# Performance work log

Measured on AMD Instinct MI355X. Metric: run time of the kernel, lower is better.

Reference implementation:

```python
import jax, jax.numpy as jnp
import numpy as np

T, H, HS, NH = 1024, 2048, 64, 32
TM, TD = 32, 64  # time-mix / time-decay LoRA dims for hidden_size != 4096


def _layernorm(x, w, b, eps=1e-5):
    mu = jnp.mean(x, axis=-1, keepdims=True)
    var = jnp.mean(jnp.square(x - mu), axis=-1, keepdims=True)
    return (x - mu) * jax.lax.rsqrt(var + eps) * w + b


def setup_inputs() -> dict:
    key = jax.random.key(0)
    ks = jax.random.split(key, 16)
    s = 0.02
    return {
        'x': jax.random.normal(ks[0], (1, T, H), jnp.float32),
        'state1': jax.random.normal(ks[1], (1, H), jnp.float32),
        'state2': jax.random.normal(ks[2], (NH, HS, HS), jnp.float32) * s,
        'ln1_w': jnp.ones((H,), jnp.float32),
        'ln1_b': jnp.zeros((H,), jnp.float32),
        'time_maa_x': jax.random.normal(ks[3], (1, 1, H), jnp.float32) * s,
        'time_maa': jax.random.normal(ks[4], (5, 1, H), jnp.float32) * s,
        'time_maa_w1': jax.random.normal(ks[5], (H, 5 * TM), jnp.float32) * s,
        'time_maa_w2': jax.random.normal(ks[6], (5, TM, H), jnp.float32) * s,
        'time_decay_w1': jax.random.normal(ks[7], (H, TD), jnp.float32) * s,
        'time_decay_w2': jax.random.normal(ks[8], (TD, H), jnp.float32) * s,
        'time_decay_p': jax.random.normal(ks[9], (NH, 1, HS), jnp.float32),
        'time_first': jax.random.normal(ks[10], (NH, 1, HS), jnp.float32) * s,
        'W_r': jax.random.normal(ks[11], (H, H), jnp.float32) * s,
        'W_k': jax.random.normal(ks[12], (H, H), jnp.float32) * s,
        'W_v': jax.random.normal(ks[13], (H, H), jnp.float32) * s,
        'W_g': jax.random.normal(ks[14], (H, H), jnp.float32) * s,
        'W_o': jax.random.normal(ks[15], (H, H), jnp.float32) * s,
        'ln_x_w': jnp.ones((H,), jnp.float32),
        'ln_x_b': jnp.zeros((H,), jnp.float32),
    }


def _forward(x, state1, state2, ln1_w, ln1_b, time_maa_x, time_maa,
             time_maa_w1, time_maa_w2, time_decay_w1, time_decay_w2,
             time_decay_p, time_first, W_r, W_k, W_v, W_g, W_o, ln_x_w, ln_x_b):
    last_x = x
    xl = _layernorm(x, ln1_w, ln1_b)                 # (1,T,H)
    Tn = xl.shape[1]
    # token shift: sx = shift(x) - x, with state1 as the t=-1 token
    past = jnp.concatenate([state1[:, None, :], xl[:, :-1, :]], axis=1)
    sx = past - xl                                    # (1,T,H)
    state1_out = xl[:, -1, :]
    # data-dependent time-mix (LoRA through w1/w2)
    xxx = xl + sx * time_maa_x                        # (1,T,H)
    t5 = jnp.tanh(xxx[0] @ time_maa_w1)               # (T,5*TM)
    t5 = t5.reshape(Tn, 5, TM).transpose(1, 0, 2)     # (5,T,TM)
    mix = jnp.einsum('ftm,fmh->fth', t5, time_maa_w2) # (5,T,H)
    x5 = xl + sx * (mix + time_maa)                   # (5,T,H)
    mw, mk, mv, mr, mg = x5[0], x5[1], x5[2], x5[3], x5[4]
    r = (mr @ W_r).reshape(Tn, NH, HS)
    k = (mk @ W_k).reshape(Tn, NH, HS)
    v = (mv @ W_v).reshape(Tn, NH, HS)
    g = jax.nn.silu(mg @ W_g)                         # (T,H)
    # data-dependent decay
    td = (jnp.tanh(mw @ time_decay_w1) @ time_decay_w2).reshape(Tn, NH, 1, HS)
    td = td + time_decay_p                            # (T,NH,1,HS)
    td = jnp.exp(-jnp.exp(jnp.clip(td, -9.72, 2.27)))
    # WKV linear-attention recurrence
    kv = jnp.einsum('thi,thj->thij', v, k)            # (T,NH,HS,HS)

    def step(s2, inp):
        kv_t, r_t, td_t = inp
        tmp = kv_t * time_first + s2                  # (NH,HS,HS)
        wkv_t = jnp.einsum('hij,hj->hi', tmp, r_t)    # (NH,HS)
        return kv_t + s2 * td_t, wkv_t

    state2_out, wkv = jax.lax.scan(step, state2, (kv, r, td))  # wkv (T,NH,HS)
    # group-norm over head dim, then affine with ln_x params at hidden width
    y = _layernorm(wkv, 1.0, 0.0).reshape(1, Tn, H)
    y = (y * ln_x_w + ln_x_b) * g[None]
    y = y @ W_o
    return last_x + y, state1_out, state2_out


def reference(x, state1, state2, ln1_w, ln1_b, time_maa_x, time_maa,
              time_maa_w1, time_maa_w2, time_decay_w1, time_decay_w2,
              time_decay_p, time_first, W_r, W_k, W_v, W_g, W_o, ln_x_w, ln_x_b):
    return _forward(x, state1, state2, ln1_w, ln1_b, time_maa_x, time_maa,
                    time_maa_w1, time_maa_w2, time_decay_w1, time_decay_w2,
                    time_decay_p, time_first, W_r, W_k, W_v, W_g, W_o, ln_x_w, ln_x_b)
```

## Files before the change

### kernel.cpp

```cpp
#include <hip/hip_runtime.h>
#include <hip/hip_bf16.h>
#include <math.h>

#define TLEN 1024
#define HDIM 2048
#define NHEAD 32
#define HSZ 64
#define THE (TLEN * HDIM)
#define NC 32
#define CT (TLEN / NC)

typedef __attribute__((ext_vector_type(8))) short bf16x8;
typedef __attribute__((ext_vector_type(4))) float f32x4;

__device__ __forceinline__ float waveRedSum(float v) {
#pragma unroll
  for (int off = 32; off > 0; off >>= 1) v += __shfl_xor(v, off, 64);
  return v;
}

__device__ __forceinline__ void gll16(const __hip_bfloat16* g, __hip_bfloat16* l) {
  __builtin_amdgcn_global_load_lds(
      (const __attribute__((address_space(1))) void*)g,
      (__attribute__((address_space(3))) void*)l, 16, 0, 0);
}

struct TrArgs {
  const float* src[8];
  __hip_bfloat16* dst[8];
  int R[8];
  int C[8];
};

__global__ __launch_bounds__(256) void transp_kernel(TrArgs ta) {
  const int z = blockIdx.z;
  const int R = ta.R[z], C = ta.C[z];
  const int c0 = blockIdx.x * 32, r0 = blockIdx.y * 32;
  if (c0 >= C || r0 >= R) return;
  __shared__ float tile[32][33];
  const int tx = threadIdx.x & 31, ty = threadIdx.x >> 5;
  const float* src = ta.src[z];
  __hip_bfloat16* dst = ta.dst[z];
#pragma unroll
  for (int i = 0; i < 4; i++)
    tile[ty + i * 8][tx] = src[(size_t)(r0 + ty + i * 8) * C + c0 + tx];
  __syncthreads();
#pragma unroll
  for (int i = 0; i < 4; i++)
    dst[(size_t)(c0 + ty + i * 8) * R + r0 + tx] = __float2bfloat16(tile[tx][ty + i * 8]);
}

__global__ __launch_bounds__(256) void ln1_kernel(const float* __restrict__ x,
                                                  const float* __restrict__ w,
                                                  const float* __restrict__ b,
                                                  float* __restrict__ xl,
                                                  float* __restrict__ s1out) {
  const int t = blockIdx.x;
  const int tid = threadIdx.x;
  const int wid = tid >> 6, lane = tid & 63;
  const float4* xr = (const float4*)(x + (size_t)t * HDIM);
  float4 a = xr[tid];
  float4 c = xr[tid + 256];
  float va[8] = {a.x, a.y, a.z, a.w, c.x, c.y, c.z, c.w};
  float sum = 0.f;
#pragma unroll
  for (int i = 0; i < 8; i++) sum += va[i];
  sum = waveRedSum(sum);
  __shared__ float red[8];
  if (lane == 0) red[wid] = sum;
  __syncthreads();
  const float mu = (red[0] + red[1] + red[2] + red[3]) * (1.f / HDIM);
  float vs = 0.f;
#pragma unroll
  for (int i = 0; i < 8; i++) { float d = va[i] - mu; vs += d * d; }
  vs = waveRedSum(vs);
  if (lane == 0) red[4 + wid] = vs;
  __syncthreads();
  const float rstd = rsqrtf((red[4] + red[5] + red[6] + red[7]) * (1.f / HDIM) + 1e-5f);
  float* xrow = xl + (size_t)t * HDIM;
#pragma unroll
  for (int i = 0; i < 8; i++) {
    const int idx = (i < 4) ? (4 * tid + i) : (1024 + 4 * tid + (i - 4));
    const float o = (va[i] - mu) * rstd * w[idx] + b[idx];
    xrow[idx] = o;
    if (t == TLEN - 1) s1out[idx] = o;
  }
}

__global__ __launch_bounds__(256) void tokshift_kernel(const float* __restrict__ xl,
                                                       const float* __restrict__ s1,
                                                       const float* __restrict__ tmx,
                                                       __hip_bfloat16* __restrict__ xxx) {
  const int t = blockIdx.x;
  const int h = blockIdx.y * 256 + threadIdx.x;
  const float cur = xl[(size_t)t * HDIM + h];
  const float past = (t > 0) ? xl[(size_t)(t - 1) * HDIM + h] : s1[h];
  xxx[(size_t)t * HDIM + h] = __float2bfloat16(cur + (past - cur) * tmx[h]);
}

__global__ __launch_bounds__(256) void mix_kernel(const float* __restrict__ t5,
                                                  const float* __restrict__ xl,
                                                  const float* __restrict__ s1,
                                                  const float* __restrict__ w2,
                                                  const float* __restrict__ maa,
                                                  __hip_bfloat16* __restrict__ x5b) {
  const int h = blockIdx.x * 256 + threadIdx.x;
  const int t0 = blockIdx.y * 8;
  __shared__ float t5L[8 * 160];
  for (int i = threadIdx.x; i < 8 * 160; i += 256) {
    const int rr = i / 160, cc = i - rr * 160;
    t5L[i] = t5[(size_t)(t0 + rr) * 160 + cc];
  }
  __syncthreads();
  float mixv[8][5];
#pragma unroll
  for (int ts = 0; ts < 8; ts++)
#pragma unroll
    for (int f = 0; f < 5; f++) mixv[ts][f] = 0.f;
#pragma unroll
  for (int f = 0; f < 5; f++) {
#pragma unroll 4
    for (int m = 0; m < 32; m++) {
      const float w2v = w2[(size_t)(f * 32 + m) * HDIM + h];
#pragma unroll
      for (int ts = 0; ts < 8; ts++) mixv[ts][f] += t5L[ts * 160 + f * 32 + m] * w2v;
    }
  }
#pragma unroll
  for (int ts = 0; ts < 8; ts++) {
    const int t = t0 + ts;
    const float cur = xl[(size_t)t * HDIM + h];
    const float past = (t > 0) ? xl[(size_t)(t - 1) * HDIM + h] : s1[h];
    const float sx = past - cur;
#pragma unroll
    for (int f = 0; f < 5; f++) {
      const float v = cur + sx * (mixv[ts][f] + maa[(size_t)f * HDIM + h]);
      x5b[(size_t)f * THE + (size_t)t * HDIM + h] = __float2bfloat16(v);
    }
  }
}

struct GemmArgs {
  const __hip_bfloat16* A[8];
  const __hip_bfloat16* B[8];
  void* C[8];
  const float* aux[8];
  int epi[8];
  int M, N, K, Ks;
};

__global__ __launch_bounds__(256) void gemm_bt(GemmArgs ga) {
  const int z = blockIdx.z;
  const __hip_bfloat16* __restrict__ A = ga.A[z];
  const __hip_bfloat16* __restrict__ Bt = ga.B[z];
  const int N = ga.N, K = ga.K, Ks = ga.Ks;
  const int epi = ga.epi[z];
  const float* __restrict__ aux = ga.aux[z];
  void* Cz = ga.C[z];

  __shared__ __align__(16) __hip_bfloat16 As[2][128 * 64];
  __shared__ __align__(16) __hip_bfloat16 Bs[2][128 * 64];

  const int tid = threadIdx.x;
  const int wid = tid >> 6;
  const int lane = tid & 63;

  int bx = blockIdx.x, by = blockIdx.y;
  if (gridDim.x == 8 && gridDim.y == 16) {
    const int flat = bx + 8 * by;
    const int xcd = flat & 7, rem = flat >> 3;
    bx = rem & 7;
    by = xcd + 8 * (rem >> 3);
  }
  const int m0 = bx * 128;
  const int n0 = by * 128;
  const int wr = wid >> 1, wc = wid & 1;

  const int srow = lane >> 3;
  const int chunkS = (lane & 7) ^ srow;
  const __hip_bfloat16* aSrcQ[4];
  const __hip_bfloat16* bSrcQ[4];
#pragma unroll
  for (int q = 0; q < 4; q++) {
    const int arow = wid * 32 + q * 8 + srow;
    int brow = n0 + arow; if (brow > N - 1) brow = N - 1;
    aSrcQ[q] = A + (size_t)(m0 + arow) * Ks + chunkS * 8;
    bSrcQ[q] = Bt + (size_t)brow * Ks + chunkS * 8;
  }

  f32x4 acc[4][4];
#pragma unroll
  for (int m = 0; m < 4; m++)
#pragma unroll
    for (int n = 0; n < 4; n++) acc[m][n] = 0.f;

  const int lr = lane & 15;
  const int cbase = lane >> 4;
  int aoffk[2], boffk[2];
#pragma unroll
  for (int kg = 0; kg < 2; kg++) {
    const int phys = (kg * 4 + cbase) ^ (lr & 7);
    aoffk[kg] = (wr * 64 + lr) * 64 + phys * 8;
    boffk[kg] = (wc * 64 + lr) * 64 + phys * 8;
  }

#define STAGE(BUF, KT)                                              \
  do {                                                              \
    _Pragma("unroll") for (int q = 0; q < 4; q++) {                 \
      gll16(aSrcQ[q] + (KT), &As[BUF][(wid * 32 + q * 8) * 64]);    \
      gll16(bSrcQ[q] + (KT), &Bs[BUF][(wid * 32 + q * 8) * 64]);    \
    }                                                               \
  } while (0)

  STAGE(0, 0);
  int cur = 0;
  for (int kt = 0; kt < K; kt += 64) {
    const bool more = (kt + 64 < K);
    if (more) {
      STAGE(cur ^ 1, kt + 64);
      asm volatile("s_waitcnt vmcnt(8)" ::: "memory");
    } else {
      asm volatile("s_waitcnt vmcnt(0)" ::: "memory");
    }
    __builtin_amdgcn_s_barrier();
#pragma unroll
    for (int kg = 0; kg < 2; kg++) {
      bf16x8 af[4], bfv[4];
#pragma unroll
      for (int m = 0; m < 4; m++) af[m] = *(const bf16x8*)&As[cur][aoffk[kg] + m * 16 * 64];
#pragma unroll
      for (int n = 0; n < 4; n++) bfv[n] = *(const bf16x8*)&Bs[cur][boffk[kg] + n * 16 * 64];
#pragma unroll
      for (int m = 0; m < 4; m++)
#pragma unroll
        for (int n = 0; n < 4; n++)
          acc[m][n] = __builtin_amdgcn_mfma_f32_16x16x32_bf16(af[m], bfv[n], acc[m][n], 0, 0, 0);
    }
    __builtin_amdgcn_s_barrier();
    cur ^= 1;
  }
#undef STAGE

  const int r4 = (lane >> 4) * 4;
#pragma unroll
  for (int m = 0; m < 4; m++) {
#pragma unroll
    for (int n = 0; n < 4; n++) {
      const int gn = n0 + wc * 64 + n * 16 + lr;
      if (gn < N) {
#pragma unroll
        for (int r = 0; r < 4; r++) {
          const int gm = m0 + wr * 64 + m * 16 + r4 + r;
          const size_t idx = (size_t)gm * N + gn;
          const float v = acc[m][n][r];
          switch (epi) {
            case 0: ((__hip_bfloat16*)Cz)[idx] = __float2bfloat16(v); break;
            case 1: ((__hip_bfloat16*)Cz)[idx] = __float2bfloat16(v / (1.f + expf(-v))); break;
            case 2: ((float*)Cz)[idx] = tanhf(v); break;
            case 3: ((__hip_bfloat16*)Cz)[idx] = __float2bfloat16(tanhf(v)); break;
            case 4: {
              float wv = v + aux[gn];
              wv = fminf(fmaxf(wv, -9.72f), 2.27f);
              ((float*)Cz)[idx] = expf(-expf(wv));
            } break;
            case 5: ((float*)Cz)[idx] = v + aux[idx]; break;
            case 6: ((float*)Cz)[idx] = v; break;
          }
        }
      }
    }
  }
}

__global__ __launch_bounds__(256) void comb8_tanh_f32(const float* __restrict__ p,
                                                      float* __restrict__ o, int n) {
  const int i = blockIdx.x * 256 + threadIdx.x;
  float s = 0.f;
#pragma unroll
  for (int k = 0; k < 8; k++) s += p[(size_t)k * n + i];
  o[i] = tanhf(s);
}

__global__ __launch_bounds__(256) void comb8_tanh_bf16(const float* __restrict__ p,
                                                       __hip_bfloat16* __restrict__ o, int n) {
  const int i = blockIdx.x * 256 + threadIdx.x;
  float s = 0.f;
#pragma unroll
  for (int k = 0; k < 8; k++) s += p[(size_t)k * n + i];
  o[i] = __float2bfloat16(tanhf(s));
}

__global__ __launch_bounds__(256) void comb2_resid(const float* __restrict__ p,
                                                   const float* __restrict__ x,
                                                   float* __restrict__ o) {
  const int i = blockIdx.x * 256 + threadIdx.x;
  const float4 a = ((const float4*)p)[i];
  const float4 b = ((const float4*)(p + THE))[i];
  const float4 c = ((const float4*)x)[i];
  ((float4*)o)[i] = make_float4(a.x + b.x + c.x, a.y + b.y + c.y,
                                a.z + b.z + c.z, a.w + b.w + c.w);
}

__global__ __launch_bounds__(64) void decay_kernel(const __hip_bfloat16* __restrict__ rb,
                                                   const float* __restrict__ td,
                                                   __hip_bfloat16* __restrict__ rt,
                                                   float* __restrict__ Ptot) {
  const int blk = blockIdx.x;
  const int c = blk >> 5, h = blk & 31;
  const int j = threadIdx.x;
  const int hb = h * HSZ;
  const int t0 = c * CT;
  float A = 1.f;
  for (int t = 0; t < CT; t++) {
    const size_t rowb = (size_t)(t0 + t) * HDIM + hb;
    rt[(((size_t)c * NHEAD + h) * CT + t) * HSZ + j] =
        __float2bfloat16(__bfloat162float(rb[rowb + j]) * A);
    A *= td[rowb + j];
  }
  Ptot[((size_t)c * NHEAD + h) * HSZ + j] = A;
}

__global__ __launch_bounds__(256) void scan_local_kernel(const __hip_bfloat16* __restrict__ kb,
                                                         const __hip_bfloat16* __restrict__ rb,
                                                         const float* __restrict__ td,
                                                         const __hip_bfloat16* __restrict__ vb,
                                                         float* __restrict__ wkv,
                                                         float* __restrict__ qT) {
  const int blk = blockIdx.x;
  const int c = blk >> 5, h = blk & 31;
  const int w = threadIdx.x >> 6;
  const int i = threadIdx.x & 63;
  __shared__ float plds[2][4][64];

  float s[16];
#pragma unroll
  for (int q = 0; q < 16; q++) s[q] = 0.f;

  const int t0 = c * CT;
  const int hb = h * HSZ;

  for (int t = 0; t < CT; t++) {
    const size_t rowb = (size_t)(t0 + t) * HDIM + hb;
    const unsigned* kw = (const unsigned*)(kb + rowb + w * 16);
    const unsigned* rw = (const unsigned*)(rb + rowb + w * 16);
    const float* tdw = td + rowb + w * 16;
    const float vi = __bfloat162float(vb[rowb + i]);
    float p = 0.f;
#pragma unroll
    for (int m = 0; m < 8; m++) {
      const unsigned kpair = kw[m];
      const unsigned rpair = rw[m];
      const float k0 = __builtin_bit_cast(float, kpair << 16);
      const float k1 = __builtin_bit_cast(float, kpair & 0xffff0000u);
      const float r0 = __builtin_bit_cast(float, rpair << 16);
      const float r1 = __builtin_bit_cast(float, rpair & 0xffff0000u);
      const float td0 = tdw[2 * m];
      const float td1 = tdw[2 * m + 1];
      const float kv0 = vi * k0;
      const float kv1 = vi * k1;
      p = fmaf(r0, s[2 * m], p);
      p = fmaf(r1, s[2 * m + 1], p);
      s[2 * m] = fmaf(s[2 * m], td0, kv0);
      s[2 * m + 1] = fmaf(s[2 * m + 1], td1, kv1);
    }
    plds[t & 1][w][i] = p;
    __syncthreads();
    if (w == 0) {
      wkv[rowb + i] = plds[t & 1][0][i] + plds[t & 1][1][i] +
                      plds[t & 1][2][i] + plds[t & 1][3][i];
    }
  }
  float* qbase = qT + (((size_t)c * NHEAD + h) * HSZ + w * 16) * HSZ + i;
#pragma unroll
  for (int q = 0; q < 16; q++) qbase[(size_t)q * HSZ] = s[q];
}

__global__ __launch_bounds__(64) void scan_s_kernel(const float* __restrict__ qT,
                                                    const float* __restrict__ Ptot,
                                                    const float* __restrict__ s2in,
                                                    __hip_bfloat16* __restrict__ s0b,
                                                    float* __restrict__ s2out) {
  const int h = blockIdx.x, i = blockIdx.y, j = threadIdx.x;
  float s = s2in[((size_t)h * HSZ + i) * HSZ + j];
#pragma unroll 4
  for (int c = 0; c < NC; c++) {
    s0b[(((size_t)c * NHEAD + h) * HSZ + i) * HSZ + j] = __float2bfloat16(s);
    s = fmaf(s, Ptot[((size_t)c * NHEAD + h) * HSZ + j],
             qT[(((size_t)c * NHEAD + h) * HSZ + j) * HSZ + i]);
  }
  s2out[((size_t)h * HSZ + i) * HSZ + j] = s;
}

__global__ __launch_bounds__(256) void corr_kernel(const __hip_bfloat16* __restrict__ rt,
                                                   const __hip_bfloat16* __restrict__ s0b,
                                                   float* __restrict__ wkv) {
  const int c = blockIdx.x, h = blockIdx.y;
  const int w = threadIdx.x >> 6;
  const int lane = threadIdx.x & 63;
  const int lr = lane & 15, lk = (lane >> 4) * 8;
  const __hip_bfloat16* rbase = rt + (((size_t)c * NHEAD + h) * CT) * HSZ;
  const __hip_bfloat16* sbase = s0b + (((size_t)c * NHEAD + h) * HSZ) * HSZ;
  float* wbase = wkv + (size_t)(c * CT) * HDIM + h * HSZ;
#pragma unroll
  for (int mt = 0; mt < CT / 16; mt++) {
    f32x4 acc = {0.f, 0.f, 0.f, 0.f};
#pragma unroll
    for (int ks = 0; ks < 2; ks++) {
      bf16x8 af = *(const bf16x8*)(rbase + (size_t)(mt * 16 + lr) * HSZ + ks * 32 + lk);
      bf16x8 bf = *(const bf16x8*)(sbase + (size_t)(w * 16 + lr) * HSZ + ks * 32 + lk);
      acc = __builtin_amdgcn_mfma_f32_16x16x32_bf16(af, bf, acc, 0, 0, 0);
    }
    const int row = mt * 16 + (lane >> 4) * 4;
    const int col = w * 16 + lr;
#pragma unroll
    for (int r = 0; r < 4; r++)
      wbase[(size_t)(row + r) * HDIM + col] += acc[r];
  }
}

__global__ __launch_bounds__(256) void gnorm_kernel(const float* __restrict__ wkv,
                                                    const __hip_bfloat16* __restrict__ kb,
                                                    const __hip_bfloat16* __restrict__ rb,
                                                    const float* __restrict__ tf,
                                                    const __hip_bfloat16* __restrict__ vb,
                                                    const __hip_bfloat16* __restrict__ gb,
                                                    const float* __restrict__ lnw,
                                                    const float* __restrict__ lnb,
                                                    __hip_bfloat16* __restrict__ yA) {
  const int t = blockIdx.x;
  const int wid = threadIdx.x >> 6, j = threadIdx.x & 63;
  const int h = blockIdx.y * 4 + wid;
  const size_t idx = (size_t)t * HDIM + h * HSZ + j;
  const float kj = __bfloat162float(kb[idx]);
  const float rj = __bfloat162float(rb[idx]);
  const float dg = waveRedSum(rj * tf[h * HSZ + j] * kj);
  const float v = wkv[idx] + dg * __bfloat162float(vb[idx]);
  const float mu = waveRedSum(v) * (1.f / HSZ);
  const float d = v - mu;
  const float var = waveRedSum(d * d) * (1.f / HSZ);
  float y = d * rsqrtf(var + 1e-5f);
  y = y * lnw[h * HSZ + j] + lnb[h * HSZ + j];
  y *= __bfloat162float(gb[idx]);
  yA[idx] = __float2bfloat16(y);
}

extern "C" void kernel_launch(void* const* d_in, const int* in_sizes, int n_in,
                              void* d_out, int out_size, void* d_ws, size_t ws_size,
                              hipStream_t stream) {
  (void)in_sizes; (void)n_in; (void)out_size; (void)ws_size;

  const float* x    = (const float*)d_in[0];
  const float* s1   = (const float*)d_in[1];
  const float* s2   = (const float*)d_in[2];
  const float* ln1w = (const float*)d_in[3];
  const float* ln1b = (const float*)d_in[4];
  const float* tmx  = (const float*)d_in[5];
  const float* tmaa = (const float*)d_in[6];
  const float* w1   = (const float*)d_in[7];
  const float* w2   = (const float*)d_in[8];
  const float* dw1  = (const float*)d_in[9];
  const float* dw2  = (const float*)d_in[10];
  const float* dp   = (const float*)d_in[11];
  const float* tf   = (const float*)d_in[12];
  const float* Wr   = (const float*)d_in[13];
  const float* Wk   = (const float*)d_in[14];
  const float* Wv   = (const float*)d_in[15];
  const float* Wg   = (const float*)d_in[16];
  const float* Wo   = (const float*)d_in[17];
  const float* lnxw = (const float*)d_in[18];
  const float* lnxb = (const float*)d_in[19];

  float* out0  = (float*)d_out;
  float* s1out = out0 + (size_t)TLEN * HDIM;
  float* s2out = s1out + HDIM;

  char* wp = (char*)d_ws;
  size_t off = 0;
  auto carve = [&](size_t bytes) -> void* {
    void* r = wp + off;
    off += (bytes + 255) & ~(size_t)255;
    return r;
  };

  __hip_bfloat16* wrt  = (__hip_bfloat16*)carve((size_t)HDIM * HDIM * 2);
  __hip_bfloat16* wkt  = (__hip_bfloat16*)carve((size_t)HDIM * HDIM * 2);
  __hip_bfloat16* wvt  = (__hip_bfloat16*)carve((size_t)HDIM * HDIM * 2);
  __hip_bfloat16* wgt  = (__hip_bfloat16*)carve((size_t)HDIM * HDIM * 2);
  __hip_bfloat16* wot  = (__hip_bfloat16*)carve((size_t)HDIM * HDIM * 2);
  __hip_bfloat16* w1t  = (__hip_bfloat16*)carve((size_t)160 * HDIM * 2);
  __hip_bfloat16* dw1t = (__hip_bfloat16*)carve((size_t)64 * HDIM * 2);
  __hip_bfloat16* dw2t = (__hip_bfloat16*)carve((size_t)HDIM * 64 * 2);
  float* xl            = (float*)carve((size_t)THE * 4);
  __hip_bfloat16* xxx  = (__hip_bfloat16*)carve((size_t)THE * 2);
  float* t5            = (float*)carve((size_t)TLEN * 160 * 4);
  __hip_bfloat16* x5b  = (__hip_bfloat16*)carve((size_t)5 * THE * 2);
  __hip_bfloat16* rb   = (__hip_bfloat16*)carve((size_t)THE * 2);
  __hip_bfloat16* kb   = (__hip_bfloat16*)carve((size_t)THE * 2);
  __hip_bfloat16* vb   = (__hip_bfloat16*)carve((size_t)THE * 2);
  __hip_bfloat16* gb   = (__hip_bfloat16*)carve((size_t)THE * 2);
  __hip_bfloat16* tw   = (__hip_bfloat16*)carve((size_t)TLEN * 64 * 2);
  float* td            = (float*)carve((size_t)THE * 4);
  float* wkv           = (float*)carve((size_t)THE * 4);
  __hip_bfloat16* yA   = (__hip_bfloat16*)carve((size_t)THE * 2);

  float* qT            = (float*)x5b;
  __hip_bfloat16* rt   = (__hip_bfloat16*)xl;
  __hip_bfloat16* s0b  = (__hip_bfloat16*)td;
  float* Ptot          = (float*)t5;
  float* pg1           = (float*)td;
  float* pg4           = (float*)xxx;
  float* pg6           = (float*)x5b;

  TrArgs ta;
  const float* srcs[8] = {Wr, Wk, Wv, Wg, Wo, w1, dw1, dw2};
  __hip_bfloat16* dsts[8] = {wrt, wkt, wvt, wgt, wot, w1t, dw1t, dw2t};
  const int Rs[8] = {HDIM, HDIM, HDIM, HDIM, HDIM, HDIM, HDIM, 64};
  const int Cs[8] = {HDIM, HDIM, HDIM, HDIM, HDIM, 160, 64, HDIM};
  for (int z = 0; z < 8; z++) { ta.src[z] = srcs[z]; ta.dst[z] = dsts[z]; ta.R[z] = Rs[z]; ta.C[z] = Cs[z]; }
  transp_kernel<<<dim3(64, 64, 8), 256, 0, stream>>>(ta);

  ln1_kernel<<<dim3(TLEN), 256, 0, stream>>>(x, ln1w, ln1b, xl, s1out);

  tokshift_kernel<<<dim3(TLEN, HDIM / 256), 256, 0, stream>>>(xl, s1, tmx, xxx);

  {
    GemmArgs g{};
    for (int ks = 0; ks < 8; ks++) {
      g.A[ks] = xxx + ks * 256;
      g.B[ks] = w1t + ks * 256;
      g.C[ks] = pg1 + (size_t)ks * TLEN * 160;
      g.epi[ks] = 6;
    }
    g.M = TLEN; g.N = 160; g.K = 256; g.Ks = HDIM;
    gemm_bt<<<dim3(TLEN / 128, 2, 8), 256, 0, stream>>>(g);
    comb8_tanh_f32<<<dim3(TLEN * 160 / 256), 256, 0, stream>>>(pg1, t5, TLEN * 160);
  }

  mix_kernel<<<dim3(HDIM / 256, TLEN / 8), 256, 0, stream>>>(t5, xl, s1, w2, tmaa, x5b);

  {
    GemmArgs g{};
    g.A[0] = x5b + (size_t)3 * THE; g.B[0] = wrt; g.C[0] = rb; g.epi[0] = 0;
    g.A[1] = x5b + (size_t)1 * THE; g.B[1] = wkt; g.C[1] = kb; g.epi[1] = 0;
    g.A[2] = x5b + (size_t)2 * THE; g.B[2] = wvt; g.C[2] = vb; g.epi[2] = 0;
    g.A[3] = x5b + (size_t)4 * THE; g.B[3] = wgt; g.C[3] = gb; g.epi[3] = 1;
    g.M = TLEN; g.N = HDIM; g.K = HDIM; g.Ks = HDIM;
    gemm_bt<<<dim3(TLEN / 128, HDIM / 128, 4), 256, 0, stream>>>(g);
  }

  {
    GemmArgs g{};
    for (int ks = 0; ks < 8; ks++) {
      g.A[ks] = x5b + ks * 256;
      g.B[ks] = dw1t + ks * 256;
      g.C[ks] = pg4 + (size_t)ks * TLEN * 64;
      g.epi[ks] = 6;
    }
    g.M = TLEN; g.N = 64; g.K = 256; g.Ks = HDIM;
    gemm_bt<<<dim3(TLEN / 128, 1, 8), 256, 0, stream>>>(g);
    comb8_tanh_bf16<<<dim3(TLEN * 64 / 256), 256, 0, stream>>>(pg4, tw, TLEN * 64);
  }

  {
    GemmArgs g{};
    g.A[0] = tw; g.B[0] = dw2t; g.C[0] = td; g.aux[0] = dp; g.epi[0] = 4;
    g.M = TLEN; g.N = HDIM; g.K = 64; g.Ks = 64;
    gemm_bt<<<dim3(TLEN / 128, HDIM / 128, 1), 256, 0, stream>>>(g);
  }

  decay_kernel<<<dim3(NC * NHEAD), 64, 0, stream>>>(rb, td, rt, Ptot);
  scan_local_kernel<<<dim3(NC * NHEAD), 256, 0, stream>>>(kb, rb, td, vb, wkv, qT);
  scan_s_kernel<<<dim3(NHEAD, HSZ), 64, 0, stream>>>(qT, Ptot, s2, s0b, s2out);
  corr_kernel<<<dim3(NC, NHEAD), 256, 0, stream>>>(rt, s0b, wkv);

  gnorm_kernel<<<dim3(TLEN, NHEAD / 4), 256, 0, stream>>>(wkv, kb, rb, tf, vb, gb, lnxw, lnxb, yA);

  {
    GemmArgs g{};
    for (int ks = 0; ks < 2; ks++) {
      g.A[ks] = yA + ks * 1024;
      g.B[ks] = wot + ks * 1024;
      g.C[ks] = pg6 + (size_t)ks * THE;
      g.epi[ks] = 6;
    }
    g.M = TLEN; g.N = HDIM; g.K = 1024; g.Ks = HDIM;
    gemm_bt<<<dim3(TLEN / 128, HDIM / 128, 2), 256, 0, stream>>>(g);
    comb2_resid<<<dim3(THE / 4 / 256), 256, 0, stream>>>(pg6, x, out0);
  }
}
```

Before: 294.0 us.

## Use triple-buffered BK=32 GEMM pipeline and split output projection four ways

The bf16 GEMM kernel moves from a double-buffered 64-wide K tile with two barriers per step to a three-stage ring of 32-wide K tiles. Each step now has one barrier and a new XOR swizzle, and loads run two stages ahead to hide latency better. The output projection is split along K into four parts instead of two, which doubles the block count for better CU occupancy. A new four-way combine kernel adds the parts and the residual. The cost is more partial-sum memory traffic and a larger partial buffer, and each step does less MFMA work per barrier.

```diff
diff --git a/kernel.cpp b/kernel.cpp
--- a/kernel.cpp
+++ b/kernel.cpp
@@ -158,8 +158,8 @@
   const float* __restrict__ aux = ga.aux[z];
   void* Cz = ga.C[z];
 
-  __shared__ __align__(16) __hip_bfloat16 As[2][128 * 64];
-  __shared__ __align__(16) __hip_bfloat16 Bs[2][128 * 64];
+  __shared__ __align__(16) __hip_bfloat16 As[3][128 * 32];
+  __shared__ __align__(16) __hip_bfloat16 Bs[3][128 * 32];
 
   const int tid = threadIdx.x;
   const int wid = tid >> 6;
@@ -176,17 +176,19 @@
   const int n0 = by * 128;
   const int wr = wid >> 1, wc = wid & 1;
 
-  const int srow = lane >> 3;
-  const int chunkS = (lane & 7) ^ srow;
-  const __hip_bfloat16* aSrcQ[4];
-  const __hip_bfloat16* bSrcQ[4];
-#pragma unroll
-  for (int q = 0; q < 4; q++) {
-    const int arow = wid * 32 + q * 8 + srow;
-    int brow = n0 + arow; if (brow > N - 1) brow = N - 1;
-    aSrcQ[q] = A + (size_t)(m0 + arow) * Ks + chunkS * 8;
-    bSrcQ[q] = Bt + (size_t)brow * Ks + chunkS * 8;
-  }
+  const int rsub = lane >> 2;
+  const int chunkS = (lane & 3) ^ ((lane >> 3) & 3);
+  const int ca = 2 * wid;
+
+  const int arow0 = ca * 16 + rsub;
+  const int arow1 = arow0 + 16;
+  int brow0 = n0 + arow0; if (brow0 > N - 1) brow0 = N - 1;
+  int brow1 = n0 + arow1; if (brow1 > N - 1) brow1 = N - 1;
+
+  const __hip_bfloat16* aSrc0 = A + (size_t)(m0 + arow0) * Ks + chunkS * 8;
+  const __hip_bfloat16* aSrc1 = A + (size_t)(m0 + arow1) * Ks + chunkS * 8;
+  const __hip_bfloat16* bSrc0 = Bt + (size_t)brow0 * Ks + chunkS * 8;
+  const __hip_bfloat16* bSrc1 = Bt + (size_t)brow1 * Ks + chunkS * 8;
 
   f32x4 acc[4][4];
 #pragma unroll
@@ -195,49 +197,45 @@
     for (int n = 0; n < 4; n++) acc[m][n] = 0.f;
 
   const int lr = lane & 15;
-  const int cbase = lane >> 4;
-  int aoffk[2], boffk[2];
-#pragma unroll
-  for (int kg = 0; kg < 2; kg++) {
-    const int phys = (kg * 4 + cbase) ^ (lr & 7);
-    aoffk[kg] = (wr * 64 + lr) * 64 + phys * 8;
-    boffk[kg] = (wc * 64 + lr) * 64 + phys * 8;
-  }
-
-#define STAGE(BUF, KT)                                              \
-  do {                                                              \
-    _Pragma("unroll") for (int q = 0; q < 4; q++) {                 \
-      gll16(aSrcQ[q] + (KT), &As[BUF][(wid * 32 + q * 8) * 64]);    \
-      gll16(bSrcQ[q] + (KT), &Bs[BUF][(wid * 32 + q * 8) * 64]);    \
-    }                                                               \
+  const int slotbase = lane >> 4;
+  const int swz = (lr >> 1) & 3;
+  const int aoff = (wr * 64 + lr) * 32 + ((slotbase ^ swz) * 8);
+  const int boff = (wc * 64 + lr) * 32 + ((slotbase ^ swz) * 8);
+
+#define STAGE(BUF, KT)                                \
+  do {                                                \
+    gll16(aSrc0 + (KT), &As[BUF][ca * 512]);          \
+    gll16(aSrc1 + (KT), &As[BUF][ca * 512 + 512]);    \
+    gll16(bSrc0 + (KT), &Bs[BUF][ca * 512]);          \
+    gll16(bSrc1 + (KT), &Bs[BUF][ca * 512 + 512]);    \
   } while (0)
 
+  const int nsteps = K >> 5;
   STAGE(0, 0);
-  int cur = 0;
-  for (int kt = 0; kt < K; kt += 64) {
-    const bool more = (kt + 64 < K);
-    if (more) {
-      STAGE(cur ^ 1, kt + 64);
-      asm volatile("s_waitcnt vmcnt(8)" ::: "memory");
+  if (nsteps > 1) STAGE(1, 32);
+  int s0 = 0;
+  for (int t = 0; t < nsteps; ++t) {
+    if (t < nsteps - 1) {
+      asm volatile("s_waitcnt vmcnt(4)" ::: "memory");
     } else {
       asm volatile("s_waitcnt vmcnt(0)" ::: "memory");
     }
     __builtin_amdgcn_s_barrier();
-#pragma unroll
-    for (int kg = 0; kg < 2; kg++) {
-      bf16x8 af[4], bfv[4];
-#pragma unroll
-      for (int m = 0; m < 4; m++) af[m] = *(const bf16x8*)&As[cur][aoffk[kg] + m * 16 * 64];
-#pragma unroll
-      for (int n = 0; n < 4; n++) bfv[n] = *(const bf16x8*)&Bs[cur][boffk[kg] + n * 16 * 64];
-#pragma unroll
-      for (int m = 0; m < 4; m++)
-#pragma unroll
-        for (int n = 0; n < 4; n++)
-          acc[m][n] = __builtin_amdgcn_mfma_f32_16x16x32_bf16(af[m], bfv[n], acc[m][n], 0, 0, 0);
-    }
-    __builtin_amdgcn_s_barrier();
-    cur ^= 1;
+    if (t + 2 < nsteps) {
+      int sw = s0 + 2; if (sw >= 3) sw -= 3;
+      STAGE(sw, (t + 2) * 32);
+    }
+    bf16x8 af[4], bfv[4];
+#pragma unroll
+    for (int m = 0; m < 4; m++) af[m] = *(const bf16x8*)&As[s0][aoff + m * 16 * 32];
+#pragma unroll
+    for (int n = 0; n < 4; n++) bfv[n] = *(const bf16x8*)&Bs[s0][boff + n * 16 * 32];
+#pragma unroll
+    for (int m = 0; m < 4; m++)
+#pragma unroll
+      for (int n = 0; n < 4; n++)
+        acc[m][n] = __builtin_amdgcn_mfma_f32_16x16x32_bf16(af[m], bfv[n], acc[m][n], 0, 0, 0);
+    s0++; if (s0 == 3) s0 = 0;
   }
 #undef STAGE
 
@@ -290,15 +288,19 @@
   o[i] = __float2bfloat16(tanhf(s));
 }
 
-__global__ __launch_bounds__(256) void comb2_resid(const float* __restrict__ p,
+__global__ __launch_bounds__(256) void comb4_resid(const float* __restrict__ p,
                                                    const float* __restrict__ x,
                                                    float* __restrict__ o) {
   const int i = blockIdx.x * 256 + threadIdx.x;
   const float4 a = ((const float4*)p)[i];
   const float4 b = ((const float4*)(p + THE))[i];
-  const float4 c = ((const float4*)x)[i];
-  ((float4*)o)[i] = make_float4(a.x + b.x + c.x, a.y + b.y + c.y,
-                                a.z + b.z + c.z, a.w + b.w + c.w);
+  const float4 c = ((const float4*)(p + 2 * (size_t)THE))[i];
+  const float4 d = ((const float4*)(p + 3 * (size_t)THE))[i];
+  const float4 e = ((const float4*)x)[i];
+  ((float4*)o)[i] = make_float4(a.x + b.x + c.x + d.x + e.x,
+                                a.y + b.y + c.y + d.y + e.y,
+                                a.z + b.z + c.z + d.z + e.z,
+                                a.w + b.w + c.w + d.w + e.w);
 }
 
 __global__ __launch_bounds__(64) void decay_kernel(const __hip_bfloat16* __restrict__ rb,
@@ -577,14 +579,14 @@
 
   {
     GemmArgs g{};
-    for (int ks = 0; ks < 2; ks++) {
-      g.A[ks] = yA + ks * 1024;
-      g.B[ks] = wot + ks * 1024;
+    for (int ks = 0; ks < 4; ks++) {
+      g.A[ks] = yA + ks * 512;
+      g.B[ks] = wot + ks * 512;
       g.C[ks] = pg6 + (size_t)ks * THE;
       g.epi[ks] = 6;
     }
-    g.M = TLEN; g.N = HDIM; g.K = 1024; g.Ks = HDIM;
-    gemm_bt<<<dim3(TLEN / 128, HDIM / 128, 2), 256, 0, stream>>>(g);
-    comb2_resid<<<dim3(THE / 4 / 256), 256, 0, stream>>>(pg6, x, out0);
-  }
-}
+    g.M = TLEN; g.N = HDIM; g.K = 512; g.Ks = HDIM;
+    gemm_bt<<<dim3(TLEN / 128, HDIM / 128, 4), 256, 0, stream>>>(g);
+    comb4_resid<<<dim3(THE / 4 / 256), 256, 0, stream>>>(pg6, x, out0);
+  }
+}
```

Result: slower. 302.8 us (+3.0%).
